# Optimization experiments

Hardware: AMD Instinct MI355X
Metric: run time of the kernel (lower is better)

The kernel has to match this reference:

```python
import jax, jax.numpy as jnp
import numpy as np

T, MEM, B, DM, N, D = 1024, 1024, 4, 1024, 16, 64
C = MEM + T
SCALE = 1.0 / D ** 0.5
LN_EPS = 1e-5


def _rel_shift(x):
    # x: [T, C, B, N] -> Transformer-XL relative shift
    t, c = x.shape[0], x.shape[1]
    zero_pad = jnp.zeros((t, 1) + x.shape[2:], x.dtype)
    x_padded = jnp.concatenate([zero_pad, x], axis=1)  # [T, C+1, B, N]
    x_padded = x_padded.reshape((c + 1, t) + x.shape[2:])
    return x_padded[1:].reshape(x.shape)


def setup_inputs() -> dict:
    key = jax.random.key(0)
    ks = jax.random.split(key, 8)
    h = jax.random.normal(ks[0], (T, B, DM), jnp.float32)
    m = jax.random.normal(ks[1], (MEM, B, DM), jnp.float32)
    r = jax.random.normal(ks[2], (C, DM), jnp.float32)
    # causal mask with memory: query i (global pos MEM+i) may attend to j <= MEM+i
    mask = (jnp.arange(C)[None, :] > (jnp.arange(T)[:, None] + MEM))[:, :, None]  # [T,C,1] bool, True=disallow
    W_qkv = jax.random.normal(ks[3], (DM, 3 * N * D), jnp.float32) * 0.02
    W_r = jax.random.normal(ks[4], (DM, N * D), jnp.float32) * 0.02
    W_o = jax.random.normal(ks[5], (N * D, DM), jnp.float32) * 0.02
    r_w_bias = jax.random.normal(ks[6], (N, D), jnp.float32)
    r_r_bias = jax.random.normal(ks[7], (N, D), jnp.float32)
    ln_gamma = jnp.ones((DM,), jnp.float32)
    ln_beta = jnp.zeros((DM,), jnp.float32)
    return {"h": h, "m": m, "r": r, "mask": mask, "W_qkv": W_qkv, "W_r": W_r,
            "W_o": W_o, "r_w_bias": r_w_bias, "r_r_bias": r_r_bias,
            "ln_gamma": ln_gamma, "ln_beta": ln_beta}


def reference(h, m, r, mask, W_qkv, W_r, W_o, r_w_bias, r_r_bias, ln_gamma, ln_beta):
    t, b = h.shape[0], h.shape[1]
    c = r.shape[0]
    cat = jnp.concatenate([m, h], axis=0)          # [C, B, DM]
    w_heads = cat @ W_qkv                           # [C, B, 3*N*D]
    w_q, w_k, w_v = jnp.split(w_heads, 3, axis=-1)
    w_q = w_q[-t:].reshape(t, b, N, D)              # [T,B,N,D]
    w_k = w_k.reshape(c, b, N, D)                   # [C,B,N,D]
    w_v = w_v.reshape(c, b, N, D)                   # [C,B,N,D]
    r_k = (r @ W_r).reshape(c, N, D)                # [C,N,D]
    AC = jnp.einsum('ibnd,jbnd->ijbn', w_q + r_w_bias, w_k)
    BD = jnp.einsum('ibnd,jnd->ijbn', w_q + r_r_bias, r_k)
    BD = _rel_shift(BD)
    score = (AC + BD) * SCALE                       # [T,C,B,N]
    score = jnp.where(mask[:, :, :, None], jnp.float32(-65000.0), score.astype(jnp.float32)).astype(score.dtype)
    prob = jax.nn.softmax(score, axis=1)
    vec = jnp.einsum('ijbn,jbnd->ibnd', prob, w_v).reshape(t, b, N * D)
    attn_out = vec @ W_o                            # [T,B,DM]
    x = h + attn_out
    mu = jnp.mean(x, axis=-1, keepdims=True)
    var = jnp.mean((x - mu) ** 2, axis=-1, keepdims=True)
    return (x - mu) * jax.lax.rsqrt(var + LN_EPS) * ln_gamma + ln_beta
```

## Files before the change

kernel.cpp:

```cpp
#include <hip/hip_runtime.h>
#include <stdint.h>

#define T_LEN 1024
#define MEM_LEN 1024
#define C_LEN 2048
#define B_SZ 4
#define DM_ 1024
#define NH 16
#define HD 64

typedef __attribute__((ext_vector_type(8))) short short8;
typedef __attribute__((ext_vector_type(4))) float f32x4;
typedef __attribute__((ext_vector_type(4))) unsigned short ushort4v;
typedef __attribute__((ext_vector_type(4))) float float4v;

__device__ __forceinline__ unsigned short f2bf(float f) {
  union { float f; unsigned int u; } v; v.f = f;
  unsigned int r = v.u + 0x7fffu + ((v.u >> 16) & 1u);
  return (unsigned short)(r >> 16);
}
__device__ __forceinline__ float bf2f(unsigned short b) {
  union { unsigned int u; float f; } v; v.u = ((unsigned int)b) << 16;
  return v.f;
}
__device__ __forceinline__ f32x4 mfma16(short8 a, short8 b, f32x4 c) {
  return __builtin_amdgcn_mfma_f32_16x16x32_bf16(a, b, c, 0, 0, 0);
}

__global__ void k_cat_convert(const float* __restrict__ m, const float* __restrict__ h,
                              unsigned short* __restrict__ outB) {
  int idx = blockIdx.x * 256 + threadIdx.x;
  const int MQ = (MEM_LEN * B_SZ * DM_) / 4;
  float4v v;
  if (idx < MQ) v = ((const float4v*)m)[idx];
  else          v = ((const float4v*)h)[idx - MQ];
  ushort4v o;
  o.x = f2bf(v.x); o.y = f2bf(v.y); o.z = f2bf(v.z); o.w = f2bf(v.w);
  ((ushort4v*)outB)[idx] = o;
}

__global__ void k_f32_to_bf16(const float* __restrict__ in, unsigned short* __restrict__ outB, int nq) {
  int idx = blockIdx.x * 256 + threadIdx.x;
  if (idx >= nq) return;
  float4v v = ((const float4v*)in)[idx];
  ushort4v o;
  o.x = f2bf(v.x); o.y = f2bf(v.y); o.z = f2bf(v.z); o.w = f2bf(v.w);
  ((ushort4v*)outB)[idx] = o;
}

__global__ void k_transpose_bf16(const float* __restrict__ in, unsigned short* __restrict__ out,
                                 int R, int Ccols) {
  __shared__ float tile[32][33];
  int c0 = blockIdx.x * 32, r0 = blockIdx.y * 32;
  int tx = threadIdx.x & 31, ty = threadIdx.x >> 5;
#pragma unroll
  for (int p = 0; p < 4; ++p)
    tile[ty + 8 * p][tx] = in[(size_t)(r0 + ty + 8 * p) * Ccols + c0 + tx];
  __syncthreads();
#pragma unroll
  for (int p = 0; p < 4; ++p)
    out[(size_t)(c0 + ty + 8 * p) * R + r0 + tx] = f2bf(tile[tx][ty + 8 * p]);
}

template <int EPI>
__global__ __launch_bounds__(256) void k_gemm(const unsigned short* __restrict__ A,
                                              const unsigned short* __restrict__ BT,
                                              void* __restrict__ Cout, int M, int N, int K) {
  __shared__ unsigned short As[128 * 64];
  __shared__ unsigned short Bs[128 * 64];
  const int tid = threadIdx.x;
  const int w = tid >> 6, l = tid & 63;
  const int wm = w >> 1, wn = w & 1;
  const int lg = l >> 4, lr = l & 15;
  const int m0 = blockIdx.y * 128, n0 = blockIdx.x * 128;
  f32x4 acc[4][4] = {};
  const int lrow8 = l >> 3;
  const int scol = (l & 7) * 8;
  const unsigned short* Abase = A + (size_t)m0 * K;
  const unsigned short* Bbase = BT + (size_t)n0 * K;
  for (int kt = 0; kt < K; kt += 64) {
    __syncthreads();
#pragma unroll
    for (int q = 0; q < 4; ++q) {
      int chunk = w * 4 + q;
      int row = chunk * 8 + lrow8;
      __builtin_amdgcn_global_load_lds(
          (const __attribute__((address_space(1))) void*)(Abase + (size_t)row * K + kt + scol),
          (__attribute__((address_space(3))) void*)(As + chunk * 512), 16, 0, 0);
      __builtin_amdgcn_global_load_lds(
          (const __attribute__((address_space(1))) void*)(Bbase + (size_t)row * K + kt + scol),
          (__attribute__((address_space(3))) void*)(Bs + chunk * 512), 16, 0, 0);
    }
    __syncthreads();
#pragma unroll
    for (int ks = 0; ks < 2; ++ks) {
      short8 a[4], bb[4];
#pragma unroll
      for (int mi = 0; mi < 4; ++mi)
        a[mi] = *(const short8*)&As[(wm * 64 + mi * 16 + lr) * 64 + ks * 32 + lg * 8];
#pragma unroll
      for (int ni = 0; ni < 4; ++ni)
        bb[ni] = *(const short8*)&Bs[(wn * 64 + ni * 16 + lr) * 64 + ks * 32 + lg * 8];
#pragma unroll
      for (int mi = 0; mi < 4; ++mi)
#pragma unroll
        for (int ni = 0; ni < 4; ++ni)
          acc[mi][ni] = mfma16(a[mi], bb[ni], acc[mi][ni]);
    }
  }
#pragma unroll
  for (int mi = 0; mi < 4; ++mi)
#pragma unroll
    for (int ni = 0; ni < 4; ++ni)
#pragma unroll
      for (int r = 0; r < 4; ++r) {
        int row = m0 + wm * 64 + mi * 16 + lg * 4 + r;
        int col = n0 + wn * 64 + ni * 16 + lr;
        if (EPI == 0)
          ((unsigned short*)Cout)[(size_t)row * N + col] = f2bf(acc[mi][ni][r]);
        else
          ((float*)Cout)[(size_t)row * N + col] = acc[mi][ni][r];
      }
}

__global__ void k_vt(const unsigned short* __restrict__ wheads, unsigned short* __restrict__ VT) {
  __shared__ unsigned short tile[64][72];
  int c0 = blockIdx.x * 64;
  int n = blockIdx.y, b = blockIdx.z;
  int t = threadIdx.x;
#pragma unroll
  for (int p = 0; p < 16; ++p) {
    int idx = p * 256 + t;
    int r = idx >> 6, d = idx & 63;
    tile[d][r] = wheads[(size_t)((c0 + r) * 4 + b) * 3072 + 2048 + n * 64 + d];
  }
  __syncthreads();
#pragma unroll
  for (int p = 0; p < 16; ++p) {
    int idx = p * 256 + t;
    int d = idx >> 6, c = idx & 63;
    VT[(size_t)((b * 16 + n) * 64 + d) * 2048 + c0 + c] = tile[d][c];
  }
}

__global__ void k_repack(const unsigned short* __restrict__ wheads,
                         const unsigned short* __restrict__ RkG,
                         unsigned short* __restrict__ Kp,
                         unsigned short* __restrict__ Qp,
                         unsigned short* __restrict__ Rkp) {
  int gid = blockIdx.x * 256 + threadIdx.x;
  const int NK = (B_SZ * NH * C_LEN * HD) / 8;
  const int NQ = (B_SZ * NH * T_LEN * HD) / 8;
  if (gid < NK) {
    int d0 = (gid & 7) * 8;
    int c  = (gid >> 3) & 2047;
    int n  = (gid >> 14) & 15;
    int b  = gid >> 18;
    short8 v = *(const short8*)&wheads[(size_t)(c * 4 + b) * 3072 + 1024 + n * 64 + d0];
    *(short8*)&Kp[(size_t)gid * 8] = v;
  } else if (gid < NK + NQ) {
    int g2 = gid - NK;
    int d0 = (g2 & 7) * 8;
    int t  = (g2 >> 3) & 1023;
    int n  = (g2 >> 13) & 15;
    int b  = g2 >> 17;
    short8 v = *(const short8*)&wheads[(size_t)((MEM_LEN + t) * 4 + b) * 3072 + n * 64 + d0];
    *(short8*)&Qp[(size_t)g2 * 8] = v;
  } else {
    int g3 = gid - NK - NQ;
    int d0 = (g3 & 7) * 8;
    int c  = (g3 >> 3) & 2047;
    int n  = g3 >> 14;
    short8 v = *(const short8*)&RkG[(size_t)c * 1024 + n * 64 + d0];
    *(short8*)&Rkp[(size_t)g3 * 8] = v;
  }
}

__global__ void k_bias_dots(const unsigned short* __restrict__ Kp,
                            const unsigned short* __restrict__ Rkp,
                            const float* __restrict__ rwb, const float* __restrict__ rrb,
                            float* __restrict__ uk, float* __restrict__ vr) {
  int gid = blockIdx.x * 256 + threadIdx.x;
  if (gid < B_SZ * NH * C_LEN) {
    int bn = gid >> 11;
    int n = bn & 15;
    const unsigned short* kp = Kp + (size_t)gid * 64;
    float s = 0.f;
#pragma unroll
    for (int q = 0; q < 8; ++q) {
      short8 v = *(const short8*)&kp[q * 8];
#pragma unroll
      for (int e = 0; e < 8; ++e)
        s += bf2f((unsigned short)v[e]) * rwb[n * 64 + q * 8 + e];
    }
    uk[gid] = s;
  } else {
    int g2 = gid - B_SZ * NH * C_LEN;
    int n = g2 >> 11;
    const unsigned short* rp = Rkp + (size_t)g2 * 64;
    float s = 0.f;
#pragma unroll
    for (int q = 0; q < 8; ++q) {
      short8 v = *(const short8*)&rp[q * 8];
#pragma unroll
      for (int e = 0; e < 8; ++e)
        s += bf2f((unsigned short)v[e]) * rrb[n * 64 + q * 8 + e];
    }
    vr[g2] = s;
  }
}

__device__ __forceinline__ void stage_tile(const unsigned short* __restrict__ Kbase,
                                           const unsigned short* __restrict__ Vbase,
                                           unsigned short* ksBuf, unsigned short* vsBuf,
                                           int j0, int tid) {
#pragma unroll
  for (int q = 0; q < 2; ++q) {
    int chunk = q * 256 + tid;
    int row = chunk >> 3;
    int slot = chunk & 7;
    int ss = slot ^ (row & 7);
    __builtin_amdgcn_global_load_lds(
        (const __attribute__((address_space(1))) void*)(Kbase + (size_t)(j0 + row) * 64 + ss * 8),
        (__attribute__((address_space(3))) void*)(ksBuf + chunk * 8), 16, 0, 0);
    __builtin_amdgcn_global_load_lds(
        (const __attribute__((address_space(1))) void*)(Vbase + (size_t)row * 2048 + j0 + ss * 8),
        (__attribute__((address_space(3))) void*)(vsBuf + chunk * 8), 16, 0, 0);
  }
}

__global__ __launch_bounds__(256) void k_attn(const unsigned short* __restrict__ Qp,
                                              const unsigned short* __restrict__ Kp,
                                              const unsigned short* __restrict__ VT,
                                              const unsigned short* __restrict__ Rkp,
                                              const float* __restrict__ uk,
                                              const float* __restrict__ vr,
                                              float* __restrict__ po,
                                              float* __restrict__ psumG) {
  __shared__ __align__(16) unsigned short Ks[2][64 * 64];
  __shared__ __align__(16) unsigned short Vs[2][64 * 64];
  __shared__ unsigned short P[4][16][72];
  const int tid = threadIdx.x;
  const int w = tid >> 6, l = tid & 63;
  const int lg = l >> 4, lr = l & 15;
  const int L = blockIdx.x;
  const int bnlo = L & 7;
  const int rest = L >> 3;
  const int bnhi = rest / 48;
  const int inner = rest - bnhi * 48;
  const int xt = inner / 3;
  const int s  = inner - xt * 3;
  const int bn = bnhi * 8 + bnlo;
  const int i0 = xt * 64;
  const int n = bn & 15, b = bn >> 4;
  const int wrow = i0 + w * 16;

  const int ntile = xt + 17;
  const int t0 = (s * ntile) / 3;
  const int t1 = ((s + 1) * ntile) / 3;

  const unsigned short* Kbase = Kp + (size_t)bn * 2048 * 64;
  const unsigned short* Vbase = VT + (size_t)bn * 64 * 2048;
  const unsigned short* Rkbase = Rkp + (size_t)n * 2048 * 64;

  short8 aq0, aq1;
  {
    const unsigned short* qp = Qp + (size_t)(bn * 1024 + wrow + lr) * 64 + lg * 8;
    aq0 = *(const short8*)qp;
    aq1 = *(const short8*)(qp + 32);
  }
  float psum[4];
  f32x4 o[4];
#pragma unroll
  for (int r = 0; r < 4; ++r) psum[r] = 0.f;
#pragma unroll
  for (int df = 0; df < 4; ++df) o[df] = (f32x4){0.f, 0.f, 0.f, 0.f};

  const float* ukp = uk + (size_t)bn * 2048;
  const float* vrp = vr + (size_t)n * 2048;

  stage_tile(Kbase, Vbase, Ks[0], Vs[0], t0 * 64, tid);
  stage_tile(Kbase, Vbase, Ks[1], Vs[1], (t0 + 1) * 64, tid);

  const float EXPC = 0.18033688011112042f;

  for (int jt = t0; jt < t1; ++jt) {
    const int j0 = jt * 64;
    const int cur = (jt - t0) & 1;
    if (jt + 1 < t1) { asm volatile("s_waitcnt vmcnt(4)" ::: "memory"); }
    else             { asm volatile("s_waitcnt vmcnt(0)" ::: "memory"); }
    __builtin_amdgcn_s_barrier();

    f32x4 sac[4];
#pragma unroll
    for (int jf = 0; jf < 4; ++jf) sac[jf] = (f32x4){0.f, 0.f, 0.f, 0.f};
#pragma unroll
    for (int jf = 0; jf < 4; ++jf) {
      int row = jf * 16 + lr;
      int rx = row & 7;
      short8 k0 = *(const short8*)&Ks[cur][row * 64 + ((lg ^ rx) * 8)];
      short8 k1 = *(const short8*)&Ks[cur][row * 64 + (((4 + lg) ^ rx) * 8)];
      sac[jf] = mfma16(aq0, k0, sac[jf]);
      sac[jf] = mfma16(aq1, k1, sac[jf]);
    }
    const int kbw = j0 + 1008 - i0 - w * 16;
    f32x4 gb[5];
#pragma unroll
    for (int jg = 0; jg < 5; ++jg) {
      int rowK = kbw + jg * 16 + lr;
      short8 b0 = {}, b1 = {};
      float vrv = 0.f;
      if (rowK < C_LEN) {
        const unsigned short* rp = Rkbase + (size_t)rowK * 64 + lg * 8;
        b0 = *(const short8*)rp;
        b1 = *(const short8*)(rp + 32);
        vrv = vrp[rowK];
      }
      f32x4 g = (f32x4){0.f, 0.f, 0.f, 0.f};
      g = mfma16(aq0, b0, g);
      g = mfma16(aq1, b1, g);
#pragma unroll
      for (int r = 0; r < 4; ++r) g[r] += vrv;
      gb[jg] = g;
    }
    float ukv[4];
#pragma unroll
    for (int jf = 0; jf < 4; ++jf) ukv[jf] = ukp[j0 + jf * 16 + lr];
    float p[4][4];
#pragma unroll
    for (int r = 0; r < 4; ++r) {
      const int R = lg * 4 + r;
      const int delta = lr + 15 - R;
      const int src = (l & 48) | (delta & 15);
      float v0 = __shfl(gb[0][r], src);
      float v1 = __shfl(gb[1][r], src);
      float v2 = __shfl(gb[2][r], src);
      float v3 = __shfl(gb[3][r], src);
      float v4 = __shfl(gb[4][r], src);
      const bool hi = delta >= 16;
      float bd0 = hi ? v1 : v0;
      float bd1 = hi ? v2 : v1;
      float bd2 = hi ? v3 : v2;
      float bd3 = hi ? v4 : v3;
      const int jlim = i0 + w * 16 + R + MEM_LEN;
      int j = j0 + lr;
      p[0][r] = (j > jlim) ? 0.f : exp2f((sac[0][r] + bd0 + ukv[0]) * EXPC);
      j += 16;
      p[1][r] = (j > jlim) ? 0.f : exp2f((sac[1][r] + bd1 + ukv[1]) * EXPC);
      j += 16;
      p[2][r] = (j > jlim) ? 0.f : exp2f((sac[2][r] + bd2 + ukv[2]) * EXPC);
      j += 16;
      p[3][r] = (j > jlim) ? 0.f : exp2f((sac[3][r] + bd3 + ukv[3]) * EXPC);
    }
#pragma unroll
    for (int jf = 0; jf < 4; ++jf)
#pragma unroll
      for (int r = 0; r < 4; ++r) psum[r] += p[jf][r];
#pragma unroll
    for (int jf = 0; jf < 4; ++jf)
#pragma unroll
      for (int r = 0; r < 4; ++r)
        P[w][lg * 4 + r][jf * 16 + lr] = f2bf(p[jf][r]);
#pragma unroll
    for (int ks = 0; ks < 2; ++ks) {
      short8 ap = *(const short8*)&P[w][lr][ks * 32 + lg * 8];
#pragma unroll
      for (int df = 0; df < 4; ++df) {
        int row = df * 16 + lr;
        int rx = row & 7;
        short8 vv = *(const short8*)&Vs[cur][row * 64 + (((ks * 4 + lg) ^ rx) * 8)];
        o[df] = mfma16(ap, vv, o[df]);
      }
    }
    __builtin_amdgcn_s_barrier();
    if (jt + 2 < t1)
      stage_tile(Kbase, Vbase, Ks[cur], Vs[cur], (jt + 2) * 64, tid);
  }
  const int pbase = (bn * 16 + xt) * 3 + s;
  float* poB = po + (size_t)pbase * 4096;
#pragma unroll
  for (int r = 0; r < 4; ++r) {
    float v = psum[r];
    v += __shfl_xor(v, 1);
    v += __shfl_xor(v, 2);
    v += __shfl_xor(v, 4);
    v += __shfl_xor(v, 8);
    if (lr == 0) psumG[pbase * 64 + w * 16 + lg * 4 + r] = v;
  }
#pragma unroll
  for (int df = 0; df < 4; ++df)
#pragma unroll
    for (int r = 0; r < 4; ++r)
      poB[(w * 16 + lg * 4 + r) * 64 + df * 16 + lr] = o[df][r];
}

__global__ __launch_bounds__(256) void k_ared(const float* __restrict__ po,
                                              const float* __restrict__ psumG,
                                              unsigned short* __restrict__ vec) {
  const int idx = blockIdx.x;
  const int tid = threadIdx.x;
  const int bn = idx >> 4, xt = idx & 15;
  const int b = bn >> 4, n = bn & 15;
  __shared__ float rs[64];
  if (tid < 64) {
    const float* q = psumG + idx * 192;
    rs[tid] = q[tid] + q[tid + 64] + q[tid + 128];
  }
  __syncthreads();
  const float4v* p0 = (const float4v*)(po + (size_t)(idx * 3 + 0) * 4096);
  const float4v* p1 = (const float4v*)(po + (size_t)(idx * 3 + 1) * 4096);
  const float4v* p2 = (const float4v*)(po + (size_t)(idx * 3 + 2) * 4096);
#pragma unroll
  for (int k = 0; k < 4; ++k) {
    int e = tid + k * 256;
    int row = e >> 4, d4 = e & 15;
    float4v a = p0[e], bb = p1[e], c = p2[e];
    float inv = 1.f / rs[row];
    int t = xt * 64 + row;
    ushort4v ov;
    ov.x = f2bf((a.x + bb.x + c.x) * inv);
    ov.y = f2bf((a.y + bb.y + c.y) * inv);
    ov.z = f2bf((a.z + bb.z + c.z) * inv);
    ov.w = f2bf((a.w + bb.w + c.w) * inv);
    *(ushort4v*)&vec[(size_t)(t * 4 + b) * 1024 + n * 64 + d4 * 4] = ov;
  }
}

__global__ __launch_bounds__(256) void k_ln(const float* __restrict__ xg, const float* __restrict__ h,
                                            const float* __restrict__ gamma, const float* __restrict__ beta,
                                            float* __restrict__ out) {
  const int row = blockIdx.x;
  const int t = threadIdx.x;
  __shared__ float red1[4], red2[4];
  float4v xv = ((const float4v*)(xg + (size_t)row * 1024))[t];
  float4v hv = ((const float4v*)(h + (size_t)row * 1024))[t];
  float x0 = xv.x + hv.x, x1 = xv.y + hv.y, x2 = xv.z + hv.z, x3 = xv.w + hv.w;
  float s = x0 + x1 + x2 + x3;
#pragma unroll
  for (int off = 1; off < 64; off <<= 1) s += __shfl_xor(s, off);
  if ((t & 63) == 0) red1[t >> 6] = s;
  __syncthreads();
  float mean = (red1[0] + red1[1] + red1[2] + red1[3]) * (1.f / 1024.f);
  float d0 = x0 - mean, d1 = x1 - mean, d2 = x2 - mean, d3 = x3 - mean;
  float q = d0 * d0 + d1 * d1 + d2 * d2 + d3 * d3;
#pragma unroll
  for (int off = 1; off < 64; off <<= 1) q += __shfl_xor(q, off);
  if ((t & 63) == 0) red2[t >> 6] = q;
  __syncthreads();
  float var = (red2[0] + red2[1] + red2[2] + red2[3]) * (1.f / 1024.f);
  float rs = rsqrtf(var + 1e-5f);
  float4v gv = ((const float4v*)gamma)[t];
  float4v bv = ((const float4v*)beta)[t];
  float4v ov;
  ov.x = d0 * rs * gv.x + bv.x;
  ov.y = d1 * rs * gv.y + bv.y;
  ov.z = d2 * rs * gv.z + bv.z;
  ov.w = d3 * rs * gv.w + bv.w;
  ((float4v*)(out + (size_t)row * 1024))[t] = ov;
}

extern "C" void kernel_launch(void* const* d_in, const int* in_sizes, int n_in,
                              void* d_out, int out_size, void* d_ws, size_t ws_size,
                              hipStream_t stream) {
  (void)in_sizes; (void)n_in; (void)out_size; (void)ws_size;
  const float* h    = (const float*)d_in[0];
  const float* m    = (const float*)d_in[1];
  const float* r    = (const float*)d_in[2];
  const float* Wqkv = (const float*)d_in[4];
  const float* Wr   = (const float*)d_in[5];
  const float* Wo   = (const float*)d_in[6];
  const float* rwb  = (const float*)d_in[7];
  const float* rrb  = (const float*)d_in[8];
  const float* gam  = (const float*)d_in[9];
  const float* bet  = (const float*)d_in[10];
  float* out = (float*)d_out;

  char* ws = (char*)d_ws;
  unsigned short* catB   = (unsigned short*)(ws + 0);
  unsigned short* WqkvT  = (unsigned short*)(ws + 16777216);
  unsigned short* WrT    = (unsigned short*)(ws + 23068672);
  unsigned short* WoT    = (unsigned short*)(ws + 25165824);
  unsigned short* wheads = (unsigned short*)(ws + 27262976);
  unsigned short* RkG    = (unsigned short*)(ws + 77594624);
  unsigned short* VT     = (unsigned short*)(ws + 81788928);
  float* uk              = (float*)(ws + 98566144);
  float* vr              = (float*)(ws + 99090432);
  unsigned short* vec    = (unsigned short*)(ws + 99221504);
  float* xbuf            = (float*)(ws + 107610112);
  unsigned short* rB     = (unsigned short*)(ws + 124387328);
  unsigned short* Kp     = (unsigned short*)(ws + 128581632);
  unsigned short* Qp     = (unsigned short*)(ws + 145358848);
  unsigned short* Rkp    = (unsigned short*)(ws + 153747456);

  float* po    = (float*)(ws + 27262976);
  float* psumG = (float*)(ws + 124387328);

  hipLaunchKernelGGL(k_cat_convert, dim3(8192), dim3(256), 0, stream, m, h, catB);
  hipLaunchKernelGGL(k_f32_to_bf16, dim3(2048), dim3(256), 0, stream, r, rB, 524288);
  hipLaunchKernelGGL(k_transpose_bf16, dim3(96, 32), dim3(256), 0, stream, Wqkv, WqkvT, 1024, 3072);
  hipLaunchKernelGGL(k_transpose_bf16, dim3(32, 32), dim3(256), 0, stream, Wr, WrT, 1024, 1024);
  hipLaunchKernelGGL(k_transpose_bf16, dim3(32, 32), dim3(256), 0, stream, Wo, WoT, 1024, 1024);
  hipLaunchKernelGGL(k_gemm<0>, dim3(24, 64), dim3(256), 0, stream, catB, WqkvT, (void*)wheads, 8192, 3072, 1024);
  hipLaunchKernelGGL(k_gemm<0>, dim3(8, 16), dim3(256), 0, stream, rB, WrT, (void*)RkG, 2048, 1024, 1024);
  hipLaunchKernelGGL(k_vt, dim3(32, 16, 4), dim3(256), 0, stream, wheads, VT);
  hipLaunchKernelGGL(k_repack, dim3(7168), dim3(256), 0, stream, wheads, RkG, Kp, Qp, Rkp);
  hipLaunchKernelGGL(k_bias_dots, dim3(640), dim3(256), 0, stream, Kp, Rkp, rwb, rrb, uk, vr);
  hipLaunchKernelGGL(k_attn, dim3(3072), dim3(256), 0, stream, Qp, Kp, VT, Rkp, uk, vr, po, psumG);
  hipLaunchKernelGGL(k_ared, dim3(1024), dim3(256), 0, stream, po, psumG, vec);
  hipLaunchKernelGGL(k_gemm<1>, dim3(8, 32), dim3(256), 0, stream, vec, WoT, (void*)xbuf, 4096, 1024, 1024);
  hipLaunchKernelGGL(k_ln, dim3(4096), dim3(256), 0, stream, xbuf, h, gam, bet, out);
}
```

Before: 357.1 us.

## Skip Q projection for memory rows and read V directly from global in attention

The QKV GEMM is split so the memory rows only compute K and V columns, while the current-segment rows compute the full Q/K/V projection. This avoids computing query projections that are never used. In the attention kernel, V tiles are no longer staged into LDS through a double buffer. Each wave instead loads its V fragments straight from global memory into registers at the start of each tile, which frees LDS and halves the async staging traffic. The risk is that the V loads are now uncached by LDS, issued per wave, and exposed in latency before the PV MFMAs.

```diff
diff --git a/kernel.cpp b/kernel.cpp
--- a/kernel.cpp
+++ b/kernel.cpp
@@ -65,7 +65,8 @@
 template <int EPI>
 __global__ __launch_bounds__(256) void k_gemm(const unsigned short* __restrict__ A,
                                               const unsigned short* __restrict__ BT,
-                                              void* __restrict__ Cout, int M, int N, int K) {
+                                              void* __restrict__ Cout, int M, int N, int K,
+                                              int ldc, int col0) {
   __shared__ unsigned short As[128 * 64];
   __shared__ unsigned short Bs[128 * 64];
   const int tid = threadIdx.x;
@@ -115,11 +116,11 @@
 #pragma unroll
       for (int r = 0; r < 4; ++r) {
         int row = m0 + wm * 64 + mi * 16 + lg * 4 + r;
-        int col = n0 + wn * 64 + ni * 16 + lr;
+        int col = col0 + n0 + wn * 64 + ni * 16 + lr;
         if (EPI == 0)
-          ((unsigned short*)Cout)[(size_t)row * N + col] = f2bf(acc[mi][ni][r]);
+          ((unsigned short*)Cout)[(size_t)row * ldc + col] = f2bf(acc[mi][ni][r]);
         else
-          ((float*)Cout)[(size_t)row * N + col] = acc[mi][ni][r];
+          ((float*)Cout)[(size_t)row * ldc + col] = acc[mi][ni][r];
       }
 }
 
@@ -210,10 +211,8 @@
   }
 }
 
-__device__ __forceinline__ void stage_tile(const unsigned short* __restrict__ Kbase,
-                                           const unsigned short* __restrict__ Vbase,
-                                           unsigned short* ksBuf, unsigned short* vsBuf,
-                                           int j0, int tid) {
+__device__ __forceinline__ void stage_k(const unsigned short* __restrict__ Kbase,
+                                        unsigned short* ksBuf, int j0, int tid) {
 #pragma unroll
   for (int q = 0; q < 2; ++q) {
     int chunk = q * 256 + tid;
@@ -223,9 +222,6 @@
     __builtin_amdgcn_global_load_lds(
         (const __attribute__((address_space(1))) void*)(Kbase + (size_t)(j0 + row) * 64 + ss * 8),
         (__attribute__((address_space(3))) void*)(ksBuf + chunk * 8), 16, 0, 0);
-    __builtin_amdgcn_global_load_lds(
-        (const __attribute__((address_space(1))) void*)(Vbase + (size_t)row * 2048 + j0 + ss * 8),
-        (__attribute__((address_space(3))) void*)(vsBuf + chunk * 8), 16, 0, 0);
   }
 }
 
@@ -238,7 +234,6 @@
                                               float* __restrict__ po,
                                               float* __restrict__ psumG) {
   __shared__ __align__(16) unsigned short Ks[2][64 * 64];
-  __shared__ __align__(16) unsigned short Vs[2][64 * 64];
   __shared__ unsigned short P[4][16][72];
   const int tid = threadIdx.x;
   const int w = tid >> 6, l = tid & 63;
@@ -279,17 +274,24 @@
   const float* ukp = uk + (size_t)bn * 2048;
   const float* vrp = vr + (size_t)n * 2048;
 
-  stage_tile(Kbase, Vbase, Ks[0], Vs[0], t0 * 64, tid);
-  stage_tile(Kbase, Vbase, Ks[1], Vs[1], (t0 + 1) * 64, tid);
+  stage_k(Kbase, Ks[0], t0 * 64, tid);
+  stage_k(Kbase, Ks[1], (t0 + 1) * 64, tid);
 
   const float EXPC = 0.18033688011112042f;
 
   for (int jt = t0; jt < t1; ++jt) {
     const int j0 = jt * 64;
     const int cur = (jt - t0) & 1;
-    if (jt + 1 < t1) { asm volatile("s_waitcnt vmcnt(4)" ::: "memory"); }
+    if (jt + 1 < t1) { asm volatile("s_waitcnt vmcnt(2)" ::: "memory"); }
     else             { asm volatile("s_waitcnt vmcnt(0)" ::: "memory"); }
     __builtin_amdgcn_s_barrier();
+
+    short8 vv[2][4];
+#pragma unroll
+    for (int ks = 0; ks < 2; ++ks)
+#pragma unroll
+      for (int df = 0; df < 4; ++df)
+        vv[ks][df] = *(const short8*)(Vbase + (size_t)(df * 16 + lr) * 2048 + j0 + ks * 32 + lg * 8);
 
     f32x4 sac[4];
 #pragma unroll
@@ -365,16 +367,12 @@
     for (int ks = 0; ks < 2; ++ks) {
       short8 ap = *(const short8*)&P[w][lr][ks * 32 + lg * 8];
 #pragma unroll
-      for (int df = 0; df < 4; ++df) {
-        int row = df * 16 + lr;
-        int rx = row & 7;
-        short8 vv = *(const short8*)&Vs[cur][row * 64 + (((ks * 4 + lg) ^ rx) * 8)];
-        o[df] = mfma16(ap, vv, o[df]);
-      }
+      for (int df = 0; df < 4; ++df)
+        o[df] = mfma16(ap, vv[ks][df], o[df]);
     }
     __builtin_amdgcn_s_barrier();
     if (jt + 2 < t1)
-      stage_tile(Kbase, Vbase, Ks[cur], Vs[cur], (jt + 2) * 64, tid);
+      stage_k(Kbase, Ks[cur], (jt + 2) * 64, tid);
   }
   const int pbase = (bn * 16 + xt) * 3 + s;
   float* poB = po + (size_t)pbase * 4096;
@@ -500,13 +498,17 @@
   hipLaunchKernelGGL(k_transpose_bf16, dim3(96, 32), dim3(256), 0, stream, Wqkv, WqkvT, 1024, 3072);
   hipLaunchKernelGGL(k_transpose_bf16, dim3(32, 32), dim3(256), 0, stream, Wr, WrT, 1024, 1024);
   hipLaunchKernelGGL(k_transpose_bf16, dim3(32, 32), dim3(256), 0, stream, Wo, WoT, 1024, 1024);
-  hipLaunchKernelGGL(k_gemm<0>, dim3(24, 64), dim3(256), 0, stream, catB, WqkvT, (void*)wheads, 8192, 3072, 1024);
-  hipLaunchKernelGGL(k_gemm<0>, dim3(8, 16), dim3(256), 0, stream, rB, WrT, (void*)RkG, 2048, 1024, 1024);
+  hipLaunchKernelGGL(k_gemm<0>, dim3(16, 64), dim3(256), 0, stream,
+                     catB, WqkvT + (size_t)1024 * 1024, (void*)wheads, 8192, 2048, 1024, 3072, 1024);
+  hipLaunchKernelGGL(k_gemm<0>, dim3(8, 32), dim3(256), 0, stream,
+                     catB + (size_t)4096 * 1024, WqkvT, (void*)(wheads + (size_t)4096 * 3072),
+                     4096, 1024, 1024, 3072, 0);
+  hipLaunchKernelGGL(k_gemm<0>, dim3(8, 16), dim3(256), 0, stream, rB, WrT, (void*)RkG, 2048, 1024, 1024, 1024, 0);
   hipLaunchKernelGGL(k_vt, dim3(32, 16, 4), dim3(256), 0, stream, wheads, VT);
   hipLaunchKernelGGL(k_repack, dim3(7168), dim3(256), 0, stream, wheads, RkG, Kp, Qp, Rkp);
   hipLaunchKernelGGL(k_bias_dots, dim3(640), dim3(256), 0, stream, Kp, Rkp, rwb, rrb, uk, vr);
   hipLaunchKernelGGL(k_attn, dim3(3072), dim3(256), 0, stream, Qp, Kp, VT, Rkp, uk, vr, po, psumG);
   hipLaunchKernelGGL(k_ared, dim3(1024), dim3(256), 0, stream, po, psumG, vec);
-  hipLaunchKernelGGL(k_gemm<1>, dim3(8, 32), dim3(256), 0, stream, vec, WoT, (void*)xbuf, 4096, 1024, 1024);
+  hipLaunchKernelGGL(k_gemm<1>, dim3(8, 32), dim3(256), 0, stream, vec, WoT, (void*)xbuf, 4096, 1024, 1024, 1024, 0);
   hipLaunchKernelGGL(k_ln, dim3(4096), dim3(256), 0, stream, xbuf, h, gam, bet, out);
 }
```

Result: slower. 463.1 us (+29.7%).
